# Kernel optimization log

Measured on AMD Instinct MI355X. Metric: run time of the kernel, lower is better.

Reference implementation:

```python
import jax, jax.numpy as jnp
import numpy as np

H = 512   # dec_hidden == enc_hidden == audio_encoder_size == input_size (forced by broadcasts)
T = 400   # decoder steps
S = 400   # alignment (encoder) frames
B = 32


def setup_inputs() -> dict:
    key = jax.random.key(0)
    ks = jax.random.split(key, 11)
    sc_h = 1.0 / np.sqrt(H)
    sc_2h = 1.0 / np.sqrt(2 * H)
    return {
        "decoder_inputs": jax.random.normal(ks[0], (T, B, H), jnp.float32),
        "alignment_inputs": jax.random.normal(ks[1], (S, B, H), jnp.float32),
        # AttentionLoop (concat): fc (H_out=H, H_in=H, no bias) + weight (H,1) -> store as (H,)
        "fc_W": jax.random.normal(ks[2], (H, H), jnp.float32) * sc_h,
        "att_w": jax.random.normal(ks[3], (H,), jnp.float32) * sc_h,
        # GRUCell(input=2H, hidden=H, bias=False); torch gate order: r, z, n
        "Wih": jax.random.normal(ks[4], (3 * H, 2 * H), jnp.float32) * sc_2h,
        "Whh": jax.random.normal(ks[5], (3 * H, H), jnp.float32) * sc_h,
        # spectral projection (H -> H, with bias)
        "spec_W": jax.random.normal(ks[6], (H, H), jnp.float32) * sc_h,
        "spec_b": jax.random.normal(ks[7], (H,), jnp.float32) * sc_h,
        # gate projection (H -> 1, with bias)
        "gate_W": jax.random.normal(ks[8], (H,), jnp.float32) * sc_h,
        "gate_b": jax.random.normal(ks[9], (1,), jnp.float32) * sc_h,
    }


def reference(decoder_inputs, alignment_inputs, fc_W, att_w, Wih, Whh,
              spec_W, spec_b, gate_W, gate_b):
    enc = alignment_inputs                      # (S, B, H)
    Tn, Bn, Hd = decoder_inputs.shape
    # teacher forcing: first decoder input is zeros (init_state), last target frame unused
    xs = jnp.concatenate(
        [jnp.zeros((1, Bn, Hd), decoder_inputs.dtype), decoder_inputs[:-1]], axis=0)

    def step(h, x):
        # additive 'concat' attention: tanh(fc(h + enc)) @ w, softmax over S
        s = jnp.tanh(jnp.einsum('sbh,eh->sbe', h + enc, fc_W))   # (S, B, H)
        e = jnp.einsum('sbe,e->sb', s, att_w)                    # (S, B)
        a = jax.nn.softmax(e, axis=0)                            # softmax over frames
        ctx = jnp.einsum('sb,sbh->bh', a, enc)                   # (B, H)
        xc = jnp.concatenate([x, ctx], axis=-1)                  # (B, 2H)
        gi = xc @ Wih.T                                          # (B, 3H)
        gh = h @ Whh.T                                           # (B, 3H)
        ir, iz, inn = jnp.split(gi, 3, axis=-1)
        hr, hz, hn = jnp.split(gh, 3, axis=-1)
        r = jax.nn.sigmoid(ir + hr)
        z = jax.nn.sigmoid(iz + hz)
        n = jnp.tanh(inn + r * hn)
        h2 = (1.0 - z) * n + z * h                               # GRUCell update
        mel = h2 @ spec_W.T + spec_b                             # (B, H)
        gate = h2 @ gate_W + gate_b                              # (B,)
        return h2, (mel, gate)

    h0 = jnp.zeros((Bn, Whh.shape[-1]), decoder_inputs.dtype)
    _, (mels, gates) = jax.lax.scan(step, h0, xs)
    # parse_decoder_outputs: stack over time then transpose(0,1)
    return mels.transpose(1, 0, 2), gates.T                      # (B,T,H), (B,T)
```

## Files before the change

kernel.cpp:

```cpp
#include <hip/hip_runtime.h>
#include <stdint.h>

typedef _Float16 half_t;
typedef _Float16 half2v __attribute__((ext_vector_type(2)));
typedef _Float16 half8v __attribute__((ext_vector_type(8)));
typedef float    f32x4  __attribute__((ext_vector_type(4)));
typedef float    f32x2  __attribute__((ext_vector_type(2)));

#define Hd 512
#define Td 400
#define Sd 400
#define Bd 32
#define HS_STR 520

#define OFF_BAR   0ull
#define OFF_HBUF  1024ull
#define OFF_PH    33792ull
#define OFF_CTXP  99328ull
#define OFF_LB    623616ull
#define ZERO_WORDS 8448
#define OFF_ENC   1048576ull
#define OFF_PENC  14155776ull
#define OFF_XS    27262976ull
#define OFF_GIX   40370176ull
#define OFF_H2A   79691776ull
#define OFF_W1    92798976ull
#define OFF_W3    94896128ull
#define OFF_WX    96468992ull
#define OFF_SPEC  98041856ull

static __device__ __forceinline__ float fast_tanh(float x){
  float t = __builtin_amdgcn_exp2f(x * 2.8853900817779268f);
  return fmaf(-2.f, __builtin_amdgcn_rcpf(t + 1.f), 1.f);
}
static __device__ __forceinline__ float fast_sigmoid(float x){
  float t = __builtin_amdgcn_exp2f(x * -1.4426950408889634f);
  return __builtin_amdgcn_rcpf(1.f + t);
}
static __device__ __forceinline__ float pade_tanh(float x){
  x = fminf(3.f, fmaxf(-3.f, x));
  float t2 = x * x;
  return (x * (27.f + t2)) * __builtin_amdgcn_rcpf(fmaf(t2, 9.f, 27.f));
}

static __device__ __forceinline__ float ld_f32_l2(const float* p){
  return __hip_atomic_load(p, __ATOMIC_RELAXED, __HIP_MEMORY_SCOPE_AGENT);
}
static __device__ __forceinline__ unsigned long long ld_u64_l2(const void* p){
  return __hip_atomic_load((const unsigned long long*)p, __ATOMIC_RELAXED,
                           __HIP_MEMORY_SCOPE_AGENT);
}

__global__ void k_init(char* ws){
  unsigned* p = (unsigned*)ws;
  int i = blockIdx.x*blockDim.x + threadIdx.x;
  if (i < ZERO_WORDS) p[i] = 0u;
}

__global__ void k_prep_enc(const float* __restrict__ src, half_t* __restrict__ dst, int n){
  int st = gridDim.x*blockDim.x;
  for (int i = blockIdx.x*blockDim.x + threadIdx.x; i < n; i += st)
    dst[i] = (half_t)src[i];
}
__global__ void k_prep_xs(const float* __restrict__ dec, half_t* __restrict__ dst){
  const int n = Td*Bd*Hd; int st = gridDim.x*blockDim.x;
  for (int i = blockIdx.x*blockDim.x + threadIdx.x; i < n; i += st){
    float v = (i < Bd*Hd) ? 0.f : dec[i - Bd*Hd];
    dst[i] = (half_t)v;
  }
}
__global__ void k_prep_w(const float* __restrict__ fcW, const float* __restrict__ Wih,
                         const float* __restrict__ Whh, const float* __restrict__ specW,
                         char* __restrict__ ws){
  half_t* w1 = (half_t*)(ws + OFF_W1);
  half_t* w3 = (half_t*)(ws + OFF_W3);
  half_t* wx = (half_t*)(ws + OFF_WX);
  half_t* sp = (half_t*)(ws + OFF_SPEC);
  int st = gridDim.x*blockDim.x;
  int t0 = blockIdx.x*blockDim.x + threadIdx.x;
  for (int i = t0; i < 2048*512; i += st)
    w1[i] = (half_t)((i < 512*512) ? fcW[i] : Whh[i - 512*512]);
  for (int i = t0; i < 1536*512; i += st){
    int r = i >> 9, k = i & 511;
    wx[i] = (half_t)Wih[r*1024 + k];
    w3[i] = (half_t)Wih[r*1024 + 512 + k];
  }
  for (int i = t0; i < 512*512; i += st) sp[i] = (half_t)specW[i];
}

template<int MODE>
__global__ __launch_bounds__(256) void k_gemm(const half_t* __restrict__ A,
                                              const half_t* __restrict__ W,
                                              void* __restrict__ out, int N,
                                              const float* __restrict__ bias)
{
  __shared__ __align__(16) half_t As[64*32];
  __shared__ __align__(16) half_t Ws[64*32];
  const int tid = threadIdx.x;
  const int m0 = blockIdx.y * 64, n0 = blockIdx.x * 64;
  const int trow = tid >> 2, tseg = tid & 3;
  const int wv = tid >> 6, ln = tid & 63;
  const int fr = ln & 15, ko = (ln >> 4) * 8;
  f32x4 acc[4];
  #pragma unroll
  for (int cb = 0; cb < 4; ++cb){ acc[cb][0]=0.f; acc[cb][1]=0.f; acc[cb][2]=0.f; acc[cb][3]=0.f; }
  for (int kk = 0; kk < 512; kk += 32){
    ((uint4*)As)[tid] = *(const uint4*)(A + (size_t)(m0 + trow)*512 + kk + tseg*8);
    ((uint4*)Ws)[tid] = *(const uint4*)(W + (size_t)(n0 + trow)*512 + kk + tseg*8);
    __syncthreads();
    half8v af = *(const half8v*)&As[(wv*16 + fr)*32 + ko];
    #pragma unroll
    for (int cb = 0; cb < 4; ++cb){
      half8v bf = *(const half8v*)&Ws[(cb*16 + fr)*32 + ko];
      acc[cb] = __builtin_amdgcn_mfma_f32_16x16x32_f16(af, bf, acc[cb], 0, 0, 0);
    }
    __syncthreads();
  }
  #pragma unroll
  for (int cb = 0; cb < 4; ++cb){
    #pragma unroll
    for (int i = 0; i < 4; ++i){
      int gr = m0 + wv*16 + (ln >> 4)*4 + i;
      int gc = n0 + cb*16 + (ln & 15);
      if (MODE == 0){
        ((half_t*)out)[(size_t)gr*N + gc] = (half_t)acc[cb][i];
      } else {
        int tt = gr >> 5, bb = gr & 31;
        ((float*)out)[(size_t)bb*(Td*Hd) + (size_t)tt*Hd + gc] = acc[cb][i] + bias[gc];
      }
    }
  }
}

__global__ __launch_bounds__(256) void k_gate(const half_t* __restrict__ h2a,
    const float* __restrict__ gW, const float* __restrict__ gb, float* __restrict__ out)
{
  const int o = blockIdx.x * 4 + (threadIdx.x >> 6);
  const int lane = threadIdx.x & 63;
  const half8v hv = *(const half8v*)(h2a + (size_t)o*512 + lane*8);
  float a = 0.f;
  #pragma unroll
  for (int i = 0; i < 8; ++i) a = fmaf((float)hv[i], gW[lane*8 + i], a);
  #pragma unroll
  for (int o2 = 1; o2 < 64; o2 <<= 1) a += __shfl_xor(a, o2);
  if (lane == 0){
    const int tt = o >> 5, bb = o & 31;
    out[Bd*Td*Hd + bb*Td + tt] = a + gb[0];
  }
}

static __device__ __forceinline__ void slot_store(unsigned* slots, int m, unsigned v){
  __hip_atomic_store(&slots[m], v, __ATOMIC_RELAXED, __HIP_MEMORY_SCOPE_AGENT);
}
static __device__ __forceinline__ void wait_slots(unsigned* slots, unsigned v){
  if (threadIdx.x < 64){
    const unsigned* sp = &slots[threadIdx.x & 31];
    for (;;){
      unsigned x = __hip_atomic_load(sp, __ATOMIC_RELAXED, __HIP_MEMORY_SCOPE_AGENT);
      if (__all((int)(x >= v))) break;
      __builtin_amdgcn_s_sleep(1);
    }
  }
  __syncthreads();
}

__global__ __launch_bounds__(512, 2) void k_main(char* __restrict__ ws,
                                                 const float* __restrict__ attw)
{
  const int g = blockIdx.x & 7;
  const int m = blockIdx.x >> 3;
  const int tid = threadIdx.x;
  const int lane = tid & 63;
  const int w = tid >> 6;
  const int b0 = g * 4;
  const int r16 = lane & 15, kg = lane >> 4;

  half_t* hbuf = (half_t*)(ws + OFF_HBUF);
  float*  ph_g = (float*)(ws + OFF_PH)   + g*2048;
  float*  ctxp = (float*)(ws + OFF_CTXP) + g*(4*8*512);
  float*  lbp  = (float*)(ws + OFF_LB)   + g*32;
  unsigned* slots = (unsigned*)(ws + OFF_BAR) + g*32;
  const half_t* Penc = (const half_t*)(ws + OFF_PENC);
  const half_t* ench = (const half_t*)(ws + OFF_ENC);
  const half_t* gix  = (const half_t*)(ws + OFF_GIX);
  half_t* h2a = (half_t*)(ws + OFF_H2A);
  const half_t* w1 = (const half_t*)(ws + OFF_W1);
  const half_t* w3 = (const half_t*)(ws + OFF_W3);

  __shared__ __align__(16) half_t PT[50*512];
  __shared__ __align__(16) half_t ETT[512*56];
  __shared__ __align__(16) half_t hs[4*HS_STR];
  __shared__ __align__(16) half_t ctxs[4*HS_STR];
  __shared__ __align__(16) float accb[8][4][16];
  __shared__ __align__(16) float ghb[3][2][4][16];
  __shared__ __align__(16) float gib[3][2][4][16];
  __shared__ __align__(16) float es[64];
  __shared__ float Ls[4];

  const int b_l = m & 3, ch = m >> 2;
  const int bglob = b0 + b_l;

  for (int i = tid; i < 50*64; i += 512){
    int s = i >> 6, c = i & 63;
    ((uint4*)PT)[s*64 + c] =
      *(const uint4*)(Penc + ((size_t)((ch*50 + s)*32 + bglob))*512 + c*8);
  }
  {
    const half_t* eb = ench + ((size_t)(ch*50)*32 + bglob)*512;
    for (int s = 0; s < 50; ++s)
      ETT[tid*56 + s] = eb[(size_t)s*16384 + tid];
  }

  half8v w1a[2];
  {
    const half_t* wr = w1 + (size_t)(m*16 + r16)*512;
    #pragma unroll
    for (int q = 0; q < 2; ++q)
      w1a[q] = *(const half8v*)(wr + (2*w+q)*32 + kg*8);
  }
  half8v wha[8], w3a[8];
  if (w < 6){
    const int gate = w >> 1, kh = w & 1;
    const half_t* wr1 = w1 + (size_t)(512 + gate*512 + m*16 + r16)*512;
    const half_t* wr3 = w3 + (size_t)(gate*512 + m*16 + r16)*512;
    #pragma unroll
    for (int i = 0; i < 8; ++i){
      wha[i] = *(const half8v*)(wr1 + (kh*8+i)*32 + kg*8);
      w3a[i] = *(const half8v*)(wr3 + (kh*8+i)*32 + kg*8);
    }
  }
  float awr[8];
  #pragma unroll
  for (int i = 0; i < 8; ++i) awr[i] = attw[lane*8 + i];

  const int s0 = (w < 6) ? 6*w : 36 + 7*(w-6);
  const int ns = (w < 6) ? 6 : 7;
  float h2keep = 0.f;
  __syncthreads();

  for (int t = 0; t < Td; ++t){
    wait_slots(slots, 3u*t);
    {
      int bb = tid >> 7, h4 = (tid & 127) * 4;
      ((unsigned long long*)hs)[bb*130 + (h4 >> 2)] =
          ld_u64_l2(((const unsigned long long*)(hbuf + b0*512)) + tid);
    }
    __syncthreads();
    {
      f32x4 acc = {0.f, 0.f, 0.f, 0.f};
      #pragma unroll
      for (int q = 0; q < 2; ++q){
        half8v bf = *(const half8v*)(hs + (lane&3)*HS_STR + (2*w+q)*32 + kg*8);
        acc = __builtin_amdgcn_mfma_f32_16x16x32_f16(w1a[q], bf, acc, 0, 0, 0);
      }
      if (r16 < 4) *((f32x4*)&accb[w][lane&3][kg*4]) = acc;
    }
    __syncthreads();
    if (tid < 64){
      const int c = tid >> 4, r = tid & 15;
      float s = 0.f;
      #pragma unroll
      for (int w2 = 0; w2 < 8; ++w2) s += accb[w2][c][r];
      ph_g[c*512 + m*16 + r] = s;
    }
    if (tid < 64){
      __asm__ __volatile__("s_waitcnt vmcnt(0)" ::: "memory");
      if (tid == 0) slot_store(slots, m, 3u*t + 1u);
    }
    if (w < 6){
      const int gate = w >> 1, kh = w & 1;
      f32x4 ga = {0.f, 0.f, 0.f, 0.f};
      #pragma unroll
      for (int i = 0; i < 8; ++i){
        half8v bf = *(const half8v*)(hs + (lane&3)*HS_STR + (kh*8+i)*32 + kg*8);
        ga = __builtin_amdgcn_mfma_f32_16x16x32_f16(wha[i], bf, ga, 0, 0, 0);
      }
      if (r16 < 4) *((f32x4*)&ghb[gate][kh][lane&3][kg*4]) = ga;
    }
    wait_slots(slots, 3u*t + 1u);
    {
      union { unsigned long long u[4]; float f[8]; } phu;
      const float* php = ph_g + b_l*512 + lane*8;
      #pragma unroll
      for (int q2 = 0; q2 < 4; ++q2)
        phu.u[q2] = ld_u64_l2(((const unsigned long long*)php) + q2);
      #pragma unroll
      for (int k = 0; k < 7; ++k){
        if (k >= ns) break;
        const int s_l = s0 + k;
        half8v pvv = *(const half8v*)(PT + s_l*512 + lane*8);
        float a = 0.f;
        #pragma unroll
        for (int i = 0; i < 8; ++i)
          a = fmaf(pade_tanh((float)pvv[i] + phu.f[i]), awr[i], a);
        #pragma unroll
        for (int o = 1; o < 64; o <<= 1) a += __shfl_xor(a, o);
        if (lane == 0) es[s_l] = a;
      }
      __syncthreads();
      if (tid < 64){
        float ev = 0.f;
        if (tid < 50){
          ev = __builtin_amdgcn_exp2f((es[tid] - 20.f) * 1.4426950408889634f);
          es[tid] = ev;
        }
        #pragma unroll
        for (int o = 1; o < 64; o <<= 1) ev += __shfl_xor(ev, o);
        if (tid == 0) lbp[b_l*8 + ch] = ev;
      }
      __syncthreads();
      const half_t* rowp = ETT + tid*56;
      float acc2 = 0.f;
      #pragma unroll
      for (int q = 0; q < 6; ++q){
        half8v r8 = *(const half8v*)(rowp + q*8);
        f32x4 ea = *(const f32x4*)&es[q*8];
        f32x4 eb2 = *(const f32x4*)&es[q*8 + 4];
        acc2 = fmaf((float)r8[0], ea[0], acc2);
        acc2 = fmaf((float)r8[1], ea[1], acc2);
        acc2 = fmaf((float)r8[2], ea[2], acc2);
        acc2 = fmaf((float)r8[3], ea[3], acc2);
        acc2 = fmaf((float)r8[4], eb2[0], acc2);
        acc2 = fmaf((float)r8[5], eb2[1], acc2);
        acc2 = fmaf((float)r8[6], eb2[2], acc2);
        acc2 = fmaf((float)r8[7], eb2[3], acc2);
      }
      acc2 = fmaf((float)rowp[48], es[48], acc2);
      acc2 = fmaf((float)rowp[49], es[49], acc2);
      ctxp[(b_l*8 + ch)*512 + tid] = acc2;
    }
    __syncthreads();
    if (tid == 0) slot_store(slots, m, 3u*t + 2u);
    float gxr = 0.f, gxz = 0.f, gxn = 0.f;
    if (tid < 64){
      const int bl = tid >> 4, jl = tid & 15;
      const int j = m*16 + jl, bg = b0 + bl;
      const half_t* gp = gix + ((size_t)t*32 + bg)*1536;
      gxr = (float)gp[j]; gxz = (float)gp[512 + j]; gxn = (float)gp[1024 + j];
    }
    wait_slots(slots, 3u*t + 2u);
    if (tid < 32){
      float v = ld_f32_l2(&lbp[tid]);
      v += __shfl_xor(v, 1); v += __shfl_xor(v, 2); v += __shfl_xor(v, 4);
      if ((tid & 7) == 0) Ls[tid >> 3] = __builtin_amdgcn_rcpf(v);
    }
    float sums[4];
    #pragma unroll
    for (int rep = 0; rep < 4; ++rep){
      float s = 0.f;
      #pragma unroll
      for (int c2 = 0; c2 < 8; ++c2)
        s += ld_f32_l2(&ctxp[(rep*8 + c2)*512 + tid]);
      sums[rep] = s;
    }
    __syncthreads();
    #pragma unroll
    for (int rep = 0; rep < 4; ++rep)
      ctxs[rep*HS_STR + tid] = (half_t)(sums[rep] * Ls[rep]);
    __syncthreads();
    if (w < 6){
      const int gate = w >> 1, kh = w & 1;
      f32x4 ia = {0.f, 0.f, 0.f, 0.f};
      #pragma unroll
      for (int i = 0; i < 8; ++i){
        half8v bf = *(const half8v*)(ctxs + (lane&3)*HS_STR + (kh*8+i)*32 + kg*8);
        ia = __builtin_amdgcn_mfma_f32_16x16x32_f16(w3a[i], bf, ia, 0, 0, 0);
      }
      if (r16 < 4) *((f32x4*)&gib[gate][kh][lane&3][kg*4]) = ia;
    }
    __syncthreads();
    if (tid < 64){
      const int bl = tid >> 4, jl = tid & 15;
      const int j = m*16 + jl, bg = b0 + bl;
      float xr = gxr + gib[0][0][bl][jl] + gib[0][1][bl][jl]
                     + ghb[0][0][bl][jl] + ghb[0][1][bl][jl];
      float xz = gxz + gib[1][0][bl][jl] + gib[1][1][bl][jl]
                     + ghb[1][0][bl][jl] + ghb[1][1][bl][jl];
      float xn = gxn + gib[2][0][bl][jl] + gib[2][1][bl][jl];
      float gnh = ghb[2][0][bl][jl] + ghb[2][1][bl][jl];
      float r = fast_sigmoid(xr);
      float z = fast_sigmoid(xz);
      float n = fast_tanh(xn + r * gnh);
      float h2v = (1.f - z) * n + z * h2keep;
      h2keep = h2v;
      hbuf[bg*512 + j] = (half_t)h2v;
      h2a[((size_t)t*32 + bg)*512 + j] = (half_t)h2v;
    }
    __syncthreads();
    if (tid == 0) slot_store(slots, m, 3u*t + 3u);
  }
}

extern "C" void kernel_launch(void* const* d_in, const int* in_sizes, int n_in,
                              void* d_out, int out_size, void* d_ws, size_t ws_size,
                              hipStream_t stream)
{
  const float* dec   = (const float*)d_in[0];
  const float* enc   = (const float*)d_in[1];
  const float* fcW   = (const float*)d_in[2];
  const float* attw  = (const float*)d_in[3];
  const float* Wih   = (const float*)d_in[4];
  const float* Whh   = (const float*)d_in[5];
  const float* specW = (const float*)d_in[6];
  const float* specb = (const float*)d_in[7];
  const float* gateW = (const float*)d_in[8];
  const float* gateb = (const float*)d_in[9];
  char* ws = (char*)d_ws;
  float* out = (float*)d_out;

  hipLaunchKernelGGL(k_init, dim3(33), dim3(256), 0, stream, ws);
  hipLaunchKernelGGL(k_prep_enc, dim3(2048), dim3(256), 0, stream,
                     enc, (half_t*)(ws + OFF_ENC), Sd*Bd*Hd);
  hipLaunchKernelGGL(k_prep_xs, dim3(2048), dim3(256), 0, stream,
                     dec, (half_t*)(ws + OFF_XS));
  hipLaunchKernelGGL(k_prep_w, dim3(1024), dim3(256), 0, stream,
                     fcW, Wih, Whh, specW, ws);
  hipLaunchKernelGGL((k_gemm<0>), dim3(8, 200), dim3(256), 0, stream,
                     (const half_t*)(ws + OFF_ENC), (const half_t*)(ws + OFF_W1),
                     (void*)(ws + OFF_PENC), 512, (const float*)nullptr);
  hipLaunchKernelGGL((k_gemm<0>), dim3(24, 200), dim3(256), 0, stream,
                     (const half_t*)(ws + OFF_XS), (const half_t*)(ws + OFF_WX),
                     (void*)(ws + OFF_GIX), 1536, (const float*)nullptr);
  hipLaunchKernelGGL(k_main, dim3(256), dim3(512), 0, stream, ws, attw);
  hipLaunchKernelGGL((k_gemm<1>), dim3(8, 200), dim3(256), 0, stream,
                     (const half_t*)(ws + OFF_H2A), (const half_t*)(ws + OFF_SPEC),
                     (void*)out, 512, specb);
  hipLaunchKernelGGL(k_gate, dim3(3200), dim3(256), 0, stream,
                     (const half_t*)(ws + OFF_H2A), gateW, gateb, out);
}
```

Baseline: 3.590 ms.

## Regroup persistent GRU kernel into 16 groups of 2 batches with dot2 matvecs

Changes the work split of the persistent recurrent kernel from 8 groups of 32 blocks (4 batches each) to 16 groups of 16 blocks (2 batches each), so each barrier involves fewer participants. The small per-step matvecs for the attention projection and GRU gates move from MFMA tiles, which were mostly padding, to register-resident weights with fdot2 and shuffle reductions. Each block now holds all three gates' weights in registers. The next step's input-gate preload is hoisted into the tail of the current step. The risks are higher register pressure and more VALU work per block, while the number of cross-block sync rounds per step stays the same.

```diff
diff --git a/kernel.cpp b/kernel.cpp
--- a/kernel.cpp
+++ b/kernel.cpp
@@ -5,20 +5,18 @@
 typedef _Float16 half2v __attribute__((ext_vector_type(2)));
 typedef _Float16 half8v __attribute__((ext_vector_type(8)));
 typedef float    f32x4  __attribute__((ext_vector_type(4)));
-typedef float    f32x2  __attribute__((ext_vector_type(2)));
 
 #define Hd 512
 #define Td 400
 #define Sd 400
 #define Bd 32
-#define HS_STR 520
 
 #define OFF_BAR   0ull
-#define OFF_HBUF  1024ull
-#define OFF_PH    33792ull
-#define OFF_CTXP  99328ull
-#define OFF_LB    623616ull
-#define ZERO_WORDS 8448
+#define OFF_HBUF  2048ull
+#define OFF_PH    34816ull
+#define OFF_CTXP  100352ull
+#define OFF_LB    624640ull
+#define ZERO_WORDS 8704
 #define OFF_ENC   1048576ull
 #define OFF_PENC  14155776ull
 #define OFF_XS    27262976ull
@@ -28,6 +26,22 @@
 #define OFF_W3    94896128ull
 #define OFF_WX    96468992ull
 #define OFF_SPEC  98041856ull
+
+#if __has_builtin(__builtin_amdgcn_fdot2)
+#define FDOT2(a,b,c) __builtin_amdgcn_fdot2((a),(b),(c),false)
+#else
+static __device__ __forceinline__ float FDOT2(half2v a, half2v b, float c){
+  return fmaf((float)a.x,(float)b.x, fmaf((float)a.y,(float)b.y,c));
+}
+#endif
+
+static __device__ __forceinline__ float dot8(half8v a, half8v b, float acc){
+  acc = FDOT2(__builtin_shufflevector(a,a,0,1), __builtin_shufflevector(b,b,0,1), acc);
+  acc = FDOT2(__builtin_shufflevector(a,a,2,3), __builtin_shufflevector(b,b,2,3), acc);
+  acc = FDOT2(__builtin_shufflevector(a,a,4,5), __builtin_shufflevector(b,b,4,5), acc);
+  acc = FDOT2(__builtin_shufflevector(a,a,6,7), __builtin_shufflevector(b,b,6,7), acc);
+  return acc;
+}
 
 static __device__ __forceinline__ float fast_tanh(float x){
   float t = __builtin_amdgcn_exp2f(x * 2.8853900817779268f);
@@ -149,12 +163,12 @@
   }
 }
 
-static __device__ __forceinline__ void slot_store(unsigned* slots, int m, unsigned v){
-  __hip_atomic_store(&slots[m], v, __ATOMIC_RELAXED, __HIP_MEMORY_SCOPE_AGENT);
+static __device__ __forceinline__ void slot_store(unsigned* slots, int r, unsigned v){
+  __hip_atomic_store(&slots[r], v, __ATOMIC_RELAXED, __HIP_MEMORY_SCOPE_AGENT);
 }
 static __device__ __forceinline__ void wait_slots(unsigned* slots, unsigned v){
   if (threadIdx.x < 64){
-    const unsigned* sp = &slots[threadIdx.x & 31];
+    const unsigned* sp = &slots[threadIdx.x & 15];
     for (;;){
       unsigned x = __hip_atomic_load(sp, __ATOMIC_RELAXED, __HIP_MEMORY_SCOPE_AGENT);
       if (__all((int)(x >= v))) break;
@@ -167,17 +181,22 @@
 __global__ __launch_bounds__(512, 2) void k_main(char* __restrict__ ws,
                                                  const float* __restrict__ attw)
 {
-  const int g = blockIdx.x & 7;
-  const int m = blockIdx.x >> 3;
+  const int bid = blockIdx.x;
+  const int ixd = bid >> 3;
+  const int r   = ixd & 15;
+  const int g   = (bid & 7)*2 + (ixd >> 4);
+  const int b0g = g*2;
   const int tid = threadIdx.x;
   const int lane = tid & 63;
-  const int w = tid >> 6;
-  const int b0 = g * 4;
-  const int r16 = lane & 15, kg = lane >> 4;
+  const int w  = tid >> 6;
+  const int rw = tid >> 4;
+  const int p  = tid & 15;
+  const int b_l = r & 1, ch = r >> 1;
+  const int bglob = b0g + b_l;
 
   half_t* hbuf = (half_t*)(ws + OFF_HBUF);
-  float*  ph_g = (float*)(ws + OFF_PH)   + g*2048;
-  float*  ctxp = (float*)(ws + OFF_CTXP) + g*(4*8*512);
+  float*  ph_g = (float*)(ws + OFF_PH)   + g*1024;
+  float*  ctxp = (float*)(ws + OFF_CTXP) + g*8192;
   float*  lbp  = (float*)(ws + OFF_LB)   + g*32;
   unsigned* slots = (unsigned*)(ws + OFF_BAR) + g*32;
   const half_t* Penc = (const half_t*)(ws + OFF_PENC);
@@ -189,16 +208,12 @@
 
   __shared__ __align__(16) half_t PT[50*512];
   __shared__ __align__(16) half_t ETT[512*56];
-  __shared__ __align__(16) half_t hs[4*HS_STR];
-  __shared__ __align__(16) half_t ctxs[4*HS_STR];
-  __shared__ __align__(16) float accb[8][4][16];
-  __shared__ __align__(16) float ghb[3][2][4][16];
-  __shared__ __align__(16) float gib[3][2][4][16];
+  __shared__ __align__(16) half_t hs[2*512];
+  __shared__ __align__(16) half_t ctxs[2*512];
+  __shared__ __align__(16) float ghb[3][2][32];
+  __shared__ __align__(16) float gib[3][2][32];
   __shared__ __align__(16) float es[64];
-  __shared__ float Ls[4];
-
-  const int b_l = m & 3, ch = m >> 2;
-  const int bglob = b0 + b_l;
+  __shared__ float Ls[2];
 
   for (int i = tid; i < 50*64; i += 512){
     int s = i >> 6, c = i & 63;
@@ -211,71 +226,73 @@
       ETT[tid*56 + s] = eb[(size_t)s*16384 + tid];
   }
 
-  half8v w1a[2];
+  half8v w1r[4], whr[3][4], w3r[3][4];
   {
-    const half_t* wr = w1 + (size_t)(m*16 + r16)*512;
-    #pragma unroll
-    for (int q = 0; q < 2; ++q)
-      w1a[q] = *(const half8v*)(wr + (2*w+q)*32 + kg*8);
-  }
-  half8v wha[8], w3a[8];
-  if (w < 6){
-    const int gate = w >> 1, kh = w & 1;
-    const half_t* wr1 = w1 + (size_t)(512 + gate*512 + m*16 + r16)*512;
-    const half_t* wr3 = w3 + (size_t)(gate*512 + m*16 + r16)*512;
-    #pragma unroll
-    for (int i = 0; i < 8; ++i){
-      wha[i] = *(const half8v*)(wr1 + (kh*8+i)*32 + kg*8);
-      w3a[i] = *(const half8v*)(wr3 + (kh*8+i)*32 + kg*8);
+    const half_t* wp = w1 + (size_t)(32*r + rw)*512 + p*32;
+    #pragma unroll
+    for (int q = 0; q < 4; ++q) w1r[q] = *(const half8v*)(wp + q*8);
+    #pragma unroll
+    for (int gate = 0; gate < 3; ++gate){
+      const half_t* wh = w1 + (size_t)(512 + gate*512 + 32*r + rw)*512 + p*32;
+      const half_t* wc = w3 + (size_t)(gate*512 + 32*r + rw)*512 + p*32;
+      #pragma unroll
+      for (int q = 0; q < 4; ++q){
+        whr[gate][q] = *(const half8v*)(wh + q*8);
+        w3r[gate][q] = *(const half8v*)(wc + q*8);
+      }
     }
   }
   float awr[8];
   #pragma unroll
   for (int i = 0; i < 8; ++i) awr[i] = attw[lane*8 + i];
 
-  const int s0 = (w < 6) ? 6*w : 36 + 7*(w-6);
-  const int ns = (w < 6) ? 6 : 7;
+  const int s0 = (w < 2) ? 7*w : 14 + 6*(w-2);
+  const int ns = (w < 2) ? 7 : 6;
   float h2keep = 0.f;
+  float gxr = 0.f, gxz = 0.f, gxn = 0.f;
+  if (tid < 64){
+    const int bl = tid >> 5, jj = tid & 31, j = 32*r + jj;
+    const half_t* gp = gix + ((size_t)(b0g + bl))*1536;
+    gxr = (float)gp[j]; gxz = (float)gp[512 + j]; gxn = (float)gp[1024 + j];
+  }
   __syncthreads();
 
   for (int t = 0; t < Td; ++t){
-    wait_slots(slots, 3u*t);
+    wait_slots(slots, 3u*(unsigned)t);
+    if (tid < 256)
+      ((unsigned long long*)hs)[tid] =
+        ld_u64_l2(((const unsigned long long*)(hbuf + b0g*512)) + tid);
+    __syncthreads();
+    half8v h8[2][4];
+    #pragma unroll
+    for (int bb = 0; bb < 2; ++bb)
+      #pragma unroll
+      for (int q = 0; q < 4; ++q)
+        h8[bb][q] = *(const half8v*)(hs + bb*512 + p*32 + q*8);
     {
-      int bb = tid >> 7, h4 = (tid & 127) * 4;
-      ((unsigned long long*)hs)[bb*130 + (h4 >> 2)] =
-          ld_u64_l2(((const unsigned long long*)(hbuf + b0*512)) + tid);
-    }
-    __syncthreads();
-    {
-      f32x4 acc = {0.f, 0.f, 0.f, 0.f};
-      #pragma unroll
-      for (int q = 0; q < 2; ++q){
-        half8v bf = *(const half8v*)(hs + (lane&3)*HS_STR + (2*w+q)*32 + kg*8);
-        acc = __builtin_amdgcn_mfma_f32_16x16x32_f16(w1a[q], bf, acc, 0, 0, 0);
-      }
-      if (r16 < 4) *((f32x4*)&accb[w][lane&3][kg*4]) = acc;
-    }
-    __syncthreads();
-    if (tid < 64){
-      const int c = tid >> 4, r = tid & 15;
-      float s = 0.f;
-      #pragma unroll
-      for (int w2 = 0; w2 < 8; ++w2) s += accb[w2][c][r];
-      ph_g[c*512 + m*16 + r] = s;
-    }
-    if (tid < 64){
-      __asm__ __volatile__("s_waitcnt vmcnt(0)" ::: "memory");
-      if (tid == 0) slot_store(slots, m, 3u*t + 1u);
-    }
-    if (w < 6){
-      const int gate = w >> 1, kh = w & 1;
-      f32x4 ga = {0.f, 0.f, 0.f, 0.f};
-      #pragma unroll
-      for (int i = 0; i < 8; ++i){
-        half8v bf = *(const half8v*)(hs + (lane&3)*HS_STR + (kh*8+i)*32 + kg*8);
-        ga = __builtin_amdgcn_mfma_f32_16x16x32_f16(wha[i], bf, ga, 0, 0, 0);
-      }
-      if (r16 < 4) *((f32x4*)&ghb[gate][kh][lane&3][kg*4]) = ga;
+      float a0 = 0.f, a1 = 0.f;
+      #pragma unroll
+      for (int q = 0; q < 4; ++q){
+        a0 = dot8(w1r[q], h8[0][q], a0);
+        a1 = dot8(w1r[q], h8[1][q], a1);
+      }
+      #pragma unroll
+      for (int o = 1; o < 16; o <<= 1){ a0 += __shfl_xor(a0, o); a1 += __shfl_xor(a1, o); }
+      if (p == 0){ ph_g[32*r + rw] = a0; ph_g[512 + 32*r + rw] = a1; }
+    }
+    __syncthreads();
+    if (tid == 0) slot_store(slots, r, 3u*t + 1u);
+    #pragma unroll
+    for (int gate = 0; gate < 3; ++gate){
+      float a0 = 0.f, a1 = 0.f;
+      #pragma unroll
+      for (int q = 0; q < 4; ++q){
+        a0 = dot8(whr[gate][q], h8[0][q], a0);
+        a1 = dot8(whr[gate][q], h8[1][q], a1);
+      }
+      #pragma unroll
+      for (int o = 1; o < 16; o <<= 1){ a0 += __shfl_xor(a0, o); a1 += __shfl_xor(a1, o); }
+      if (p == 0){ ghb[gate][0][rw] = a0; ghb[gate][1][rw] = a1; }
     }
     wait_slots(slots, 3u*t + 1u);
     {
@@ -314,80 +331,72 @@
       #pragma unroll
       for (int q = 0; q < 6; ++q){
         half8v r8 = *(const half8v*)(rowp + q*8);
-        f32x4 ea = *(const f32x4*)&es[q*8];
-        f32x4 eb2 = *(const f32x4*)&es[q*8 + 4];
-        acc2 = fmaf((float)r8[0], ea[0], acc2);
-        acc2 = fmaf((float)r8[1], ea[1], acc2);
-        acc2 = fmaf((float)r8[2], ea[2], acc2);
-        acc2 = fmaf((float)r8[3], ea[3], acc2);
-        acc2 = fmaf((float)r8[4], eb2[0], acc2);
-        acc2 = fmaf((float)r8[5], eb2[1], acc2);
-        acc2 = fmaf((float)r8[6], eb2[2], acc2);
-        acc2 = fmaf((float)r8[7], eb2[3], acc2);
+        #pragma unroll
+        for (int e = 0; e < 8; ++e) acc2 = fmaf((float)r8[e], es[q*8 + e], acc2);
       }
       acc2 = fmaf((float)rowp[48], es[48], acc2);
       acc2 = fmaf((float)rowp[49], es[49], acc2);
       ctxp[(b_l*8 + ch)*512 + tid] = acc2;
     }
     __syncthreads();
-    if (tid == 0) slot_store(slots, m, 3u*t + 2u);
-    float gxr = 0.f, gxz = 0.f, gxn = 0.f;
-    if (tid < 64){
-      const int bl = tid >> 4, jl = tid & 15;
-      const int j = m*16 + jl, bg = b0 + bl;
-      const half_t* gp = gix + ((size_t)t*32 + bg)*1536;
-      gxr = (float)gp[j]; gxz = (float)gp[512 + j]; gxn = (float)gp[1024 + j];
-    }
+    if (tid == 0) slot_store(slots, r, 3u*t + 2u);
     wait_slots(slots, 3u*t + 2u);
-    if (tid < 32){
+    if (tid < 16){
       float v = ld_f32_l2(&lbp[tid]);
       v += __shfl_xor(v, 1); v += __shfl_xor(v, 2); v += __shfl_xor(v, 4);
       if ((tid & 7) == 0) Ls[tid >> 3] = __builtin_amdgcn_rcpf(v);
     }
-    float sums[4];
-    #pragma unroll
-    for (int rep = 0; rep < 4; ++rep){
-      float s = 0.f;
-      #pragma unroll
-      for (int c2 = 0; c2 < 8; ++c2)
-        s += ld_f32_l2(&ctxp[(rep*8 + c2)*512 + tid]);
-      sums[rep] = s;
-    }
-    __syncthreads();
-    #pragma unroll
-    for (int rep = 0; rep < 4; ++rep)
-      ctxs[rep*HS_STR + tid] = (half_t)(sums[rep] * Ls[rep]);
-    __syncthreads();
-    if (w < 6){
-      const int gate = w >> 1, kh = w & 1;
-      f32x4 ia = {0.f, 0.f, 0.f, 0.f};
-      #pragma unroll
-      for (int i = 0; i < 8; ++i){
-        half8v bf = *(const half8v*)(ctxs + (lane&3)*HS_STR + (kh*8+i)*32 + kg*8);
-        ia = __builtin_amdgcn_mfma_f32_16x16x32_f16(w3a[i], bf, ia, 0, 0, 0);
-      }
-      if (r16 < 4) *((f32x4*)&gib[gate][kh][lane&3][kg*4]) = ia;
+    float sum0 = 0.f, sum1 = 0.f;
+    #pragma unroll
+    for (int c2 = 0; c2 < 8; ++c2){
+      sum0 += ld_f32_l2(&ctxp[c2*512 + tid]);
+      sum1 += ld_f32_l2(&ctxp[4096 + c2*512 + tid]);
+    }
+    __syncthreads();
+    ctxs[tid]       = (half_t)(sum0 * Ls[0]);
+    ctxs[512 + tid] = (half_t)(sum1 * Ls[1]);
+    __syncthreads();
+    {
+      half8v c8[2][4];
+      #pragma unroll
+      for (int bb = 0; bb < 2; ++bb)
+        #pragma unroll
+        for (int q = 0; q < 4; ++q)
+          c8[bb][q] = *(const half8v*)(ctxs + bb*512 + p*32 + q*8);
+      #pragma unroll
+      for (int gate = 0; gate < 3; ++gate){
+        float a0 = 0.f, a1 = 0.f;
+        #pragma unroll
+        for (int q = 0; q < 4; ++q){
+          a0 = dot8(w3r[gate][q], c8[0][q], a0);
+          a1 = dot8(w3r[gate][q], c8[1][q], a1);
+        }
+        #pragma unroll
+        for (int o = 1; o < 16; o <<= 1){ a0 += __shfl_xor(a0, o); a1 += __shfl_xor(a1, o); }
+        if (p == 0){ gib[gate][0][rw] = a0; gib[gate][1][rw] = a1; }
+      }
     }
     __syncthreads();
     if (tid < 64){
-      const int bl = tid >> 4, jl = tid & 15;
-      const int j = m*16 + jl, bg = b0 + bl;
-      float xr = gxr + gib[0][0][bl][jl] + gib[0][1][bl][jl]
-                     + ghb[0][0][bl][jl] + ghb[0][1][bl][jl];
-      float xz = gxz + gib[1][0][bl][jl] + gib[1][1][bl][jl]
-                     + ghb[1][0][bl][jl] + ghb[1][1][bl][jl];
-      float xn = gxn + gib[2][0][bl][jl] + gib[2][1][bl][jl];
-      float gnh = ghb[2][0][bl][jl] + ghb[2][1][bl][jl];
-      float r = fast_sigmoid(xr);
-      float z = fast_sigmoid(xz);
-      float n = fast_tanh(xn + r * gnh);
+      const int bl = tid >> 5, jj = tid & 31;
+      const int j = 32*r + jj, bg = b0g + bl;
+      float xr = gxr + gib[0][bl][jj] + ghb[0][bl][jj];
+      float xz = gxz + gib[1][bl][jj] + ghb[1][bl][jj];
+      float xn = gxn + gib[2][bl][jj];
+      float gnh = ghb[2][bl][jj];
+      float rr = fast_sigmoid(xr);
+      float z  = fast_sigmoid(xz);
+      float n  = fast_tanh(xn + rr * gnh);
       float h2v = (1.f - z) * n + z * h2keep;
       h2keep = h2v;
       hbuf[bg*512 + j] = (half_t)h2v;
       h2a[((size_t)t*32 + bg)*512 + j] = (half_t)h2v;
-    }
-    __syncthreads();
-    if (tid == 0) slot_store(slots, m, 3u*t + 3u);
+      const int tn = (t + 1 < Td) ? t + 1 : t;
+      const half_t* gp = gix + ((size_t)tn*32 + bg)*1536;
+      gxr = (float)gp[j]; gxz = (float)gp[512 + j]; gxn = (float)gp[1024 + j];
+    }
+    __syncthreads();
+    if (tid == 0) slot_store(slots, r, 3u*t + 3u);
   }
 }
 
@@ -408,7 +417,7 @@
   char* ws = (char*)d_ws;
   float* out = (float*)d_out;
 
-  hipLaunchKernelGGL(k_init, dim3(33), dim3(256), 0, stream, ws);
+  hipLaunchKernelGGL(k_init, dim3(34), dim3(256), 0, stream, ws);
   hipLaunchKernelGGL(k_prep_enc, dim3(2048), dim3(256), 0, stream,
                      enc, (half_t*)(ws + OFF_ENC), Sd*Bd*Hd);
   hipLaunchKernelGGL(k_prep_xs, dim3(2048), dim3(256), 0, stream,
```

Measured after the change: 3.786 ms. 1.05x slower.
